# Performance work log

Hardware: AMD Instinct MI355X
Metric: run time of the kernel (lower is better)

The kernel has to match this reference:

```python
import jax, jax.numpy as jnp
import numpy as np

# Qwen3-VL-MoE text experts (training path): token permute -> grouped GEMM
# (gate_up) -> SwiGLU -> grouped GEMM (down) -> token unpermute + prob combine.
# Routing is generated perfectly balanced (each expert receives exactly M/E
# expanded tokens) so the grouped GEMM over the sorted token buffer is exactly
# a batched matmul over E contiguous groups -- same math as npu_grouped_matmul.

E, H, D, T, K = 32, 2048, 768, 4096, 8  # experts, hidden, moe_intermediate, tokens, top_k
M = T * K                                # expanded rows


def setup_inputs() -> dict:
    key = jax.random.key(0)
    k1, k2, k3, k4, k5 = jax.random.split(key, 5)
    hidden_states = jax.random.normal(k1, (T, H), dtype=jnp.float32)
    routing_weights = jax.nn.softmax(jax.random.normal(k2, (T, E), dtype=jnp.float32), axis=-1)
    # balanced expert assignment: each expert id appears exactly M // E times
    flat = jnp.tile(jnp.arange(E, dtype=jnp.int32), M // E)
    router_indices = jax.random.permutation(k3, flat).reshape(T, K)
    gate_up_proj = jax.random.normal(k4, (E, H, 2 * D), dtype=jnp.float32) * 0.02
    down_proj = jax.random.normal(k5, (E, D, H), dtype=jnp.float32) * 0.02
    return {
        "hidden_states": hidden_states,
        "routing_weights": routing_weights,
        "router_indices": router_indices,
        "gate_up_proj": gate_up_proj,
        "down_proj": down_proj,
    }


def reference(hidden_states, routing_weights, router_indices, gate_up_proj, down_proj):
    n_tok, hid = hidden_states.shape
    n_exp = gate_up_proj.shape[0]
    top_k = router_indices.shape[1]
    n_rows = n_tok * top_k
    grp = n_rows // n_exp  # balanced group size

    # --- npu_moe_token_permute: sort expanded (token, slot) rows by expert id
    flat_experts = router_indices.reshape(-1)            # (M,)
    order = jnp.argsort(flat_experts)                    # stable sort by expert
    permuted = hidden_states[order // top_k]             # (M, H)

    # --- grouped GEMM #1 (gate_up): balanced groups -> batched matmul
    xg = permuted.reshape(n_exp, grp, hid)               # (E, g, H)
    gate_up = jnp.einsum('egh,ehd->egd', xg, gate_up_proj)  # (E, g, 2D)

    # --- npu_swiglu(dim=-1): silu(first half) * second half
    gate, up = jnp.split(gate_up, 2, axis=-1)
    act = jax.nn.silu(gate) * up                         # (E, g, D)

    # --- grouped GEMM #2 (down)
    out = jnp.einsum('egd,edh->egh', act, down_proj).reshape(n_rows, hid)

    # --- npu_moe_token_unpermute: invert permutation, combine with probs
    inv = jnp.argsort(order)
    expanded = out[inv].reshape(n_tok, top_k, hid)       # (T, K, H)
    probs = jnp.take_along_axis(routing_weights, router_indices, axis=1)  # (T, K)
    return jnp.einsum('tkh,tk->th', expanded, probs)     # (T, H)
```

## Files before the change

### kernel.cpp

```cpp
#include <hip/hip_runtime.h>
#include <hip/hip_bf16.h>
#include <cstdint>


#define E_   32
#define H_   2048
#define D_   768
#define T_   4096
#define K_   8
#define M_   (T_ * K_)
#define G_   (M_ / E_)
#define GU2  (2 * D_)

typedef unsigned short u16;
typedef short bf16x8 __attribute__((ext_vector_type(8)));
typedef float f32x4 __attribute__((ext_vector_type(4)));
typedef unsigned short u16x2 __attribute__((ext_vector_type(2)));
typedef unsigned short u16x8 __attribute__((ext_vector_type(8)));

__device__ __forceinline__ u16 f2bf(float f) {
  unsigned u = __float_as_uint(f);
  u += 0x7FFFu + ((u >> 16) & 1u);
  return (u16)(u >> 16);
}
__device__ __forceinline__ float bf2f(u16 v) {
  return __uint_as_float(((unsigned)v) << 16);
}

#define GLOAD16(g, l) __builtin_amdgcn_global_load_lds(                        \
    (const __attribute__((address_space(1))) void*)(g),                        \
    (__attribute__((address_space(3))) void*)(l), 16, 0, 0)

#define VM4()   asm volatile("s_waitcnt vmcnt(4)" ::: "memory")
#define VM0()   asm volatile("s_waitcnt vmcnt(0)" ::: "memory")
#define LGKM0() asm volatile("s_waitcnt lgkmcnt(0)" ::: "memory")
#define SCHB()  __builtin_amdgcn_sched_barrier(0)
#define BAR()   __builtin_amdgcn_s_barrier()

__global__ __launch_bounds__(256) void cvt_hidden(const float* __restrict__ in,
                                                  u16* __restrict__ out) {
  const int i = blockIdx.x * 256 + threadIdx.x;
  const float4 v = ((const float4*)in)[i];
  u16x2 a; a.x = f2bf(v.x); a.y = f2bf(v.y);
  u16x2 b; b.x = f2bf(v.z); b.y = f2bf(v.w);
  *(u16x2*)&out[(size_t)i * 4]     = a;
  *(u16x2*)&out[(size_t)i * 4 + 2] = b;
}

__global__ __launch_bounds__(256) void transpose_cvt(const float* __restrict__ in,
                                                     u16* __restrict__ out,
                                                     int R, int C, int mode) {
  __shared__ u16 tl[64][65];
  const int b = blockIdx.z;
  const int c0 = blockIdx.x * 64, r0 = blockIdx.y * 64;
  const float* ip = in + ((size_t)b * R + r0) * C + c0;
  const int lr = threadIdx.x >> 6;
  const int lc = threadIdx.x & 63;
#pragma unroll
  for (int p = 0; p < 16; ++p) {
    const int r = p * 4 + lr;
    tl[r][lc] = f2bf(ip[(size_t)r * C + lc]);
  }
  __syncthreads();
  const int wr = threadIdx.x >> 5;
  const int wi = threadIdx.x & 31;
#pragma unroll
  for (int p = 0; p < 8; ++p) {
    const int c = p * 8 + wr;
    const int gc = c0 + c;
    int rr;
    if (mode == 1) {
      const int j = (gc < D_) ? gc : (gc - D_);
      rr = (j >> 4) * 32 + ((gc < D_) ? 0 : 16) + (j & 15);
    } else {
      rr = gc;
    }
    u16x2 v; v.x = tl[2 * wi][c]; v.y = tl[2 * wi + 1][c];
    *(u16x2*)&out[((size_t)b * C + rr) * R + r0 + 2 * wi] = v;
  }
}

__global__ __launch_bounds__(256) void build_perm(const int* __restrict__ ridx,
                                                  int* __restrict__ perm_src) {
  const int e = blockIdx.x;
  const int lane = threadIdx.x & 63, wid = threadIdx.x >> 6;
  __shared__ int wcnt[4];
  __shared__ int running;
  if (threadIdx.x == 0) running = 0;
  __syncthreads();
  for (int base = 0; base < M_; base += 256) {
    const int i = base + threadIdx.x;
    const bool match = (ridx[i] == e);
    const unsigned long long mask = __ballot(match);
    if (lane == 0) wcnt[wid] = __popcll(mask);
    __syncthreads();
    int wpre = 0;
    for (int w0 = 0; w0 < wid; ++w0) wpre += wcnt[w0];
    const int rank = __popcll(mask & ((1ull << lane) - 1ull));
    if (match) perm_src[e * G_ + running + wpre + rank] = i;
    __syncthreads();
    if (threadIdx.x == 0) running += wcnt[0] + wcnt[1] + wcnt[2] + wcnt[3];
    __syncthreads();
  }
}

__global__ __launch_bounds__(256) void gather_probs(const int* __restrict__ ridx,
                                                    const float* __restrict__ rw,
                                                    float* __restrict__ probs) {
  const int i = blockIdx.x * 256 + threadIdx.x;
  const int t = i >> 3;
  probs[i] = rw[t * E_ + ridx[i]];
}

__global__ __launch_bounds__(512, 2) void gemm1_swiglu(
    const u16* __restrict__ hid, const u16* __restrict__ gup,
    const int* __restrict__ perm, u16* __restrict__ act) {
  __shared__ u16 As[4][8192];
  __shared__ u16 Bs[4][8192];
  const int NT = H_ / 32;

  const int nwg = 6 * 4 * E_;
  const int wid = (blockIdx.x % 8) * (nwg / 8) + blockIdx.x / 8;
  const int e = wid / 24;
  const int mb = (wid / 6) % 4;
  const int nb = wid % 6;

  const int tid = threadIdx.x;
  const int lane = tid & 63, w = tid >> 6;
  const int wr = w >> 2, wc = w & 3;

  const int srow = tid >> 2, schunk = tid & 3;
  const u16* pA[2]; const u16* pB[2];
#pragma unroll
  for (int q = 0; q < 2; ++q) {
    const int r = q * 128 + srow;
    const int cg = (schunk ^ ((r >> 1) & 3)) * 8;
    const int token = perm[e * G_ + mb * 256 + r] >> 3;
    pA[q] = hid + (size_t)token * H_ + cg;
    pB[q] = gup + ((size_t)e * GU2 + nb * 256 + r) * H_ + cg;
  }

  int aoff[8], boff[4];
  {
    const int l15 = lane & 15, hk = lane >> 4;
#pragma unroll
    for (int m = 0; m < 8; ++m) {
      const int rA = wr * 128 + m * 16 + l15;
      aoff[m] = rA * 32 + ((hk ^ ((rA >> 1) & 3)) * 8);
    }
#pragma unroll
    for (int n = 0; n < 4; ++n) {
      const int rB = wc * 64 + n * 16 + l15;
      boff[n] = rB * 32 + ((hk ^ ((rB >> 1) & 3)) * 8);
    }
  }

  f32x4 acc[8][4];
#pragma unroll
  for (int m = 0; m < 8; ++m)
#pragma unroll
    for (int n = 0; n < 4; ++n) acc[m][n] = (f32x4){0.f, 0.f, 0.f, 0.f};

  GLOAD16(pA[0], &As[0][tid * 8]);      GLOAD16(pA[1], &As[0][4096 + tid * 8]);
  GLOAD16(pB[0], &Bs[0][tid * 8]);      GLOAD16(pB[1], &Bs[0][4096 + tid * 8]);
  GLOAD16(pA[0] + 32, &As[1][tid * 8]); GLOAD16(pA[1] + 32, &As[1][4096 + tid * 8]);
  GLOAD16(pB[0] + 32, &Bs[1][tid * 8]); GLOAD16(pB[1] + 32, &Bs[1][4096 + tid * 8]);
  VM4(); BAR(); SCHB();

#pragma unroll 4
  for (int t = 0; t < NT; ++t) {
    const int slot = t & 3, ts = (t + 2) & 3;
    const bool st = (t + 2) < NT;
    const u16* Ab = As[slot]; const u16* Bb = Bs[slot];
    bf16x8 av[4], bv[4];
#pragma unroll
    for (int n = 0; n < 4; ++n) bv[n] = *(const bf16x8*)&Bb[boff[n]];
#pragma unroll
    for (int m = 0; m < 4; ++m) av[m] = *(const bf16x8*)&Ab[aoff[m]];
    if (st) {
      GLOAD16(pA[0] + (t + 2) * 32, &As[ts][tid * 8]);
      GLOAD16(pA[1] + (t + 2) * 32, &As[ts][4096 + tid * 8]);
    }
    SCHB(); BAR(); LGKM0(); SCHB();
    __builtin_amdgcn_s_setprio(1);
#pragma unroll
    for (int m = 0; m < 4; ++m)
#pragma unroll
      for (int n = 0; n < 4; ++n)
        acc[m][n] = __builtin_amdgcn_mfma_f32_16x16x32_bf16(av[m], bv[n],
                                                            acc[m][n], 0, 0, 0);
    __builtin_amdgcn_s_setprio(0);
    SCHB(); BAR();
#pragma unroll
    for (int m = 0; m < 4; ++m) av[m] = *(const bf16x8*)&Ab[aoff[m + 4]];
    if (st) {
      GLOAD16(pB[0] + (t + 2) * 32, &Bs[ts][tid * 8]);
      GLOAD16(pB[1] + (t + 2) * 32, &Bs[ts][4096 + tid * 8]);
    }
    SCHB(); BAR(); LGKM0(); SCHB();
    __builtin_amdgcn_s_setprio(1);
#pragma unroll
    for (int m = 0; m < 4; ++m)
#pragma unroll
      for (int n = 0; n < 4; ++n)
        acc[m + 4][n] = __builtin_amdgcn_mfma_f32_16x16x32_bf16(av[m], bv[n],
                                                                acc[m + 4][n], 0, 0, 0);
    __builtin_amdgcn_s_setprio(0);
    SCHB();
    if (st) { VM4(); } else { VM0(); }
    BAR();
  }

  const int lrow = (lane >> 4) * 4, lcol = lane & 15;
#pragma unroll
  for (int m = 0; m < 8; ++m)
#pragma unroll
    for (int p = 0; p < 2; ++p)
#pragma unroll
      for (int r = 0; r < 4; ++r) {
        const float g = acc[m][2 * p][r];
        const float u = acc[m][2 * p + 1][r];
        const float a_ = g / (1.f + __expf(-g)) * u;
        const int row = mb * 256 + wr * 128 + m * 16 + lrow + r;
        const int dcol = (nb * 8 + wc * 2 + p) * 16 + lcol;
        act[((size_t)e * G_ + row) * D_ + dcol] = f2bf(a_);
      }
}

__global__ __launch_bounds__(512, 2) void gemm2_scatter(
    const u16* __restrict__ act, const u16* __restrict__ dwn,
    const int* __restrict__ perm, u16* __restrict__ expo) {
  __shared__ u16 As[4][8192];
  __shared__ u16 Bs[4][8192];
  const int NT = D_ / 32;

  const int nwg = 8 * 4 * E_;
  const int wid = (blockIdx.x % 8) * (nwg / 8) + blockIdx.x / 8;
  const int e = wid / 32;
  const int mb = (wid / 8) % 4;
  const int nb = wid % 8;

  const int tid = threadIdx.x;
  const int lane = tid & 63, w = tid >> 6;
  const int wr = w >> 2, wc = w & 3;

  const int srow = tid >> 2, schunk = tid & 3;
  const u16* pA[2]; const u16* pB[2];
#pragma unroll
  for (int q = 0; q < 2; ++q) {
    const int r = q * 128 + srow;
    const int cg = (schunk ^ ((r >> 1) & 3)) * 8;
    pA[q] = act + ((size_t)e * G_ + mb * 256 + r) * D_ + cg;
    pB[q] = dwn + ((size_t)e * H_ + nb * 256 + r) * D_ + cg;
  }

  int aoff[8], boff[4];
  {
    const int l15 = lane & 15, hk = lane >> 4;
#pragma unroll
    for (int m = 0; m < 8; ++m) {
      const int rA = wr * 128 + m * 16 + l15;
      aoff[m] = rA * 32 + ((hk ^ ((rA >> 1) & 3)) * 8);
    }
#pragma unroll
    for (int n = 0; n < 4; ++n) {
      const int rB = wc * 64 + n * 16 + l15;
      boff[n] = rB * 32 + ((hk ^ ((rB >> 1) & 3)) * 8);
    }
  }

  f32x4 acc[8][4];
#pragma unroll
  for (int m = 0; m < 8; ++m)
#pragma unroll
    for (int n = 0; n < 4; ++n) acc[m][n] = (f32x4){0.f, 0.f, 0.f, 0.f};

  GLOAD16(pA[0], &As[0][tid * 8]);      GLOAD16(pA[1], &As[0][4096 + tid * 8]);
  GLOAD16(pB[0], &Bs[0][tid * 8]);      GLOAD16(pB[1], &Bs[0][4096 + tid * 8]);
  GLOAD16(pA[0] + 32, &As[1][tid * 8]); GLOAD16(pA[1] + 32, &As[1][4096 + tid * 8]);
  GLOAD16(pB[0] + 32, &Bs[1][tid * 8]); GLOAD16(pB[1] + 32, &Bs[1][4096 + tid * 8]);
  VM4(); BAR(); SCHB();

#pragma unroll 4
  for (int t = 0; t < NT; ++t) {
    const int slot = t & 3, ts = (t + 2) & 3;
    const bool st = (t + 2) < NT;
    const u16* Ab = As[slot]; const u16* Bb = Bs[slot];
    bf16x8 av[4], bv[4];
#pragma unroll
    for (int n = 0; n < 4; ++n) bv[n] = *(const bf16x8*)&Bb[boff[n]];
#pragma unroll
    for (int m = 0; m < 4; ++m) av[m] = *(const bf16x8*)&Ab[aoff[m]];
    if (st) {
      GLOAD16(pA[0] + (t + 2) * 32, &As[ts][tid * 8]);
      GLOAD16(pA[1] + (t + 2) * 32, &As[ts][4096 + tid * 8]);
    }
    SCHB(); BAR(); LGKM0(); SCHB();
    __builtin_amdgcn_s_setprio(1);
#pragma unroll
    for (int m = 0; m < 4; ++m)
#pragma unroll
      for (int n = 0; n < 4; ++n)
        acc[m][n] = __builtin_amdgcn_mfma_f32_16x16x32_bf16(av[m], bv[n],
                                                            acc[m][n], 0, 0, 0);
    __builtin_amdgcn_s_setprio(0);
    SCHB(); BAR();
#pragma unroll
    for (int m = 0; m < 4; ++m) av[m] = *(const bf16x8*)&Ab[aoff[m + 4]];
    if (st) {
      GLOAD16(pB[0] + (t + 2) * 32, &Bs[ts][tid * 8]);
      GLOAD16(pB[1] + (t + 2) * 32, &Bs[ts][4096 + tid * 8]);
    }
    SCHB(); BAR(); LGKM0(); SCHB();
    __builtin_amdgcn_s_setprio(1);
#pragma unroll
    for (int m = 0; m < 4; ++m)
#pragma unroll
      for (int n = 0; n < 4; ++n)
        acc[m + 4][n] = __builtin_amdgcn_mfma_f32_16x16x32_bf16(av[m], bv[n],
                                                                acc[m + 4][n], 0, 0, 0);
    __builtin_amdgcn_s_setprio(0);
    SCHB();
    if (st) { VM4(); } else { VM0(); }
    BAR();
  }

  const int lrow = (lane >> 4) * 4, lcol = lane & 15;
#pragma unroll
  for (int m = 0; m < 8; ++m)
#pragma unroll
    for (int r = 0; r < 4; ++r) {
      const int dst = e * G_ + mb * 256 + wr * 128 + m * 16 + lrow + r;
      const int src = perm[dst];
      u16* orow = expo + (size_t)src * H_ + nb * 256 + wc * 64;
#pragma unroll
      for (int n = 0; n < 4; ++n)
        orow[n * 16 + lcol] = f2bf(acc[m][n][r]);
    }
}

__global__ __launch_bounds__(256) void combine(const u16* __restrict__ expo,
                                               const float* __restrict__ probs,
                                               float* __restrict__ out) {
  const int t = blockIdx.x;
  const int h0 = threadIdx.x * 8;
  float r[8] = {0.f, 0.f, 0.f, 0.f, 0.f, 0.f, 0.f, 0.f};
#pragma unroll
  for (int k = 0; k < K_; ++k) {
    const float p = probs[t * K_ + k];
    const u16x8 v = *(const u16x8*)&expo[((size_t)(t * K_ + k)) * H_ + h0];
#pragma unroll
    for (int j = 0; j < 8; ++j) r[j] += p * bf2f(v[j]);
  }
  float4 o0 = {r[0], r[1], r[2], r[3]};
  float4 o1 = {r[4], r[5], r[6], r[7]};
  *(float4*)&out[(size_t)t * H_ + h0]     = o0;
  *(float4*)&out[(size_t)t * H_ + h0 + 4] = o1;
}

extern "C" void kernel_launch(void* const* d_in, const int* in_sizes, int n_in,
                              void* d_out, int out_size, void* d_ws, size_t ws_size,
                              hipStream_t stream) {
  const float* hidden = (const float*)d_in[0];
  const float* rw     = (const float*)d_in[1];
  const int*   ridx   = (const int*)d_in[2];
  const float* gup_f  = (const float*)d_in[3];
  const float* dwn_f  = (const float*)d_in[4];
  float* out = (float*)d_out;

  char* ws = (char*)d_ws;
  size_t off = 0;
  auto alloc = [&](size_t bytes) -> void* {
    void* p = ws + off;
    off += (bytes + 255) & ~(size_t)255;
    return p;
  };
  u16*   hid_bf = (u16*)alloc((size_t)T_ * H_ * 2);
  u16*   gup_t  = (u16*)alloc((size_t)E_ * GU2 * H_ * 2);
  u16*   dwn_t  = (u16*)alloc((size_t)E_ * H_ * D_ * 2);
  u16*   act    = (u16*)alloc((size_t)M_ * D_ * 2);
  u16*   expo   = (u16*)alloc((size_t)M_ * H_ * 2);
  int*   perm   = (int*)alloc((size_t)M_ * 4);
  float* probs  = (float*)alloc((size_t)M_ * 4);
  if (off > ws_size) return;

  cvt_hidden<<<(T_ * H_ / 4) / 256, 256, 0, stream>>>(hidden, hid_bf);
  transpose_cvt<<<dim3(GU2 / 64, H_ / 64, E_), 256, 0, stream>>>(gup_f, gup_t, H_, GU2, 1);
  transpose_cvt<<<dim3(H_ / 64, D_ / 64, E_), 256, 0, stream>>>(dwn_f, dwn_t, D_, H_, 0);
  build_perm<<<E_, 256, 0, stream>>>(ridx, perm);
  gather_probs<<<M_ / 256, 256, 0, stream>>>(ridx, rw, probs);
  gemm1_swiglu<<<6 * 4 * E_, 512, 0, stream>>>(hid_bf, gup_t, perm, act);
  gemm2_scatter<<<8 * 4 * E_, 512, 0, stream>>>(act, dwn_t, perm, expo);
  combine<<<T_, 256, 0, stream>>>(expo, probs, out);
}
```

Before: 620.0 us.

## Deepen GEMM prefetch to three stages and vectorize transpose-convert kernel

Both grouped GEMM kernels now prefetch three K-tiles ahead instead of two, using the fourth LDS ring slot, with waitcnt thresholds adjusted so up to eight loads stay in flight. This is meant to hide more global memory latency behind the MFMA work. Separately, the weight transpose-convert kernel now reads float4 rows, stores transposed into a padded LDS tile, and writes 16-byte vectors instead of 4-byte pairs. The deeper pipeline adds more outstanding loads and more complex tail waits.

```diff
diff --git a/kernel.cpp b/kernel.cpp
--- a/kernel.cpp
+++ b/kernel.cpp
@@ -31,6 +31,7 @@
     (const __attribute__((address_space(1))) void*)(g),                        \
     (__attribute__((address_space(3))) void*)(l), 16, 0, 0)
 
+#define VM8()   asm volatile("s_waitcnt vmcnt(8)" ::: "memory")
 #define VM4()   asm volatile("s_waitcnt vmcnt(4)" ::: "memory")
 #define VM0()   asm volatile("s_waitcnt vmcnt(0)" ::: "memory")
 #define LGKM0() asm volatile("s_waitcnt lgkmcnt(0)" ::: "memory")
@@ -50,23 +51,27 @@
 __global__ __launch_bounds__(256) void transpose_cvt(const float* __restrict__ in,
                                                      u16* __restrict__ out,
                                                      int R, int C, int mode) {
-  __shared__ u16 tl[64][65];
+  __shared__ u16 tl[64 * 72];
   const int b = blockIdx.z;
   const int c0 = blockIdx.x * 64, r0 = blockIdx.y * 64;
+  const int tid = threadIdx.x;
   const float* ip = in + ((size_t)b * R + r0) * C + c0;
-  const int lr = threadIdx.x >> 6;
-  const int lc = threadIdx.x & 63;
-#pragma unroll
-  for (int p = 0; p < 16; ++p) {
-    const int r = p * 4 + lr;
-    tl[r][lc] = f2bf(ip[(size_t)r * C + lc]);
+  const int rr4 = tid >> 4;
+  const int cc4 = (tid & 15) * 4;
+#pragma unroll
+  for (int p = 0; p < 4; ++p) {
+    const int r = p * 16 + rr4;
+    const float4 v = *(const float4*)&ip[(size_t)r * C + cc4];
+    tl[(cc4 + 0) * 72 + r] = f2bf(v.x);
+    tl[(cc4 + 1) * 72 + r] = f2bf(v.y);
+    tl[(cc4 + 2) * 72 + r] = f2bf(v.z);
+    tl[(cc4 + 3) * 72 + r] = f2bf(v.w);
   }
   __syncthreads();
-  const int wr = threadIdx.x >> 5;
-  const int wi = threadIdx.x & 31;
-#pragma unroll
-  for (int p = 0; p < 8; ++p) {
-    const int c = p * 8 + wr;
+  const int rs = (tid & 7) * 8;
+#pragma unroll
+  for (int q = 0; q < 2; ++q) {
+    const int c = q * 32 + (tid >> 3);
     const int gc = c0 + c;
     int rr;
     if (mode == 1) {
@@ -75,8 +80,8 @@
     } else {
       rr = gc;
     }
-    u16x2 v; v.x = tl[2 * wi][c]; v.y = tl[2 * wi + 1][c];
-    *(u16x2*)&out[((size_t)b * C + rr) * R + r0 + 2 * wi] = v;
+    const u16x8 v = *(const u16x8*)&tl[c * 72 + rs];
+    *(u16x8*)&out[((size_t)b * C + rr) * R + r0 + rs] = v;
   }
 }
 
@@ -165,12 +170,14 @@
   GLOAD16(pB[0], &Bs[0][tid * 8]);      GLOAD16(pB[1], &Bs[0][4096 + tid * 8]);
   GLOAD16(pA[0] + 32, &As[1][tid * 8]); GLOAD16(pA[1] + 32, &As[1][4096 + tid * 8]);
   GLOAD16(pB[0] + 32, &Bs[1][tid * 8]); GLOAD16(pB[1] + 32, &Bs[1][4096 + tid * 8]);
-  VM4(); BAR(); SCHB();
+  GLOAD16(pA[0] + 64, &As[2][tid * 8]); GLOAD16(pA[1] + 64, &As[2][4096 + tid * 8]);
+  GLOAD16(pB[0] + 64, &Bs[2][tid * 8]); GLOAD16(pB[1] + 64, &Bs[2][4096 + tid * 8]);
+  VM8(); BAR(); SCHB();
 
 #pragma unroll 4
   for (int t = 0; t < NT; ++t) {
-    const int slot = t & 3, ts = (t + 2) & 3;
-    const bool st = (t + 2) < NT;
+    const int slot = t & 3, ts = (t + 3) & 3;
+    const bool st = (t + 3) < NT;
     const u16* Ab = As[slot]; const u16* Bb = Bs[slot];
     bf16x8 av[4], bv[4];
 #pragma unroll
@@ -178,8 +185,8 @@
 #pragma unroll
     for (int m = 0; m < 4; ++m) av[m] = *(const bf16x8*)&Ab[aoff[m]];
     if (st) {
-      GLOAD16(pA[0] + (t + 2) * 32, &As[ts][tid * 8]);
-      GLOAD16(pA[1] + (t + 2) * 32, &As[ts][4096 + tid * 8]);
+      GLOAD16(pA[0] + (t + 3) * 32, &As[ts][tid * 8]);
+      GLOAD16(pA[1] + (t + 3) * 32, &As[ts][4096 + tid * 8]);
     }
     SCHB(); BAR(); LGKM0(); SCHB();
     __builtin_amdgcn_s_setprio(1);
@@ -194,8 +201,8 @@
 #pragma unroll
     for (int m = 0; m < 4; ++m) av[m] = *(const bf16x8*)&Ab[aoff[m + 4]];
     if (st) {
-      GLOAD16(pB[0] + (t + 2) * 32, &Bs[ts][tid * 8]);
-      GLOAD16(pB[1] + (t + 2) * 32, &Bs[ts][4096 + tid * 8]);
+      GLOAD16(pB[0] + (t + 3) * 32, &Bs[ts][tid * 8]);
+      GLOAD16(pB[1] + (t + 3) * 32, &Bs[ts][4096 + tid * 8]);
     }
     SCHB(); BAR(); LGKM0(); SCHB();
     __builtin_amdgcn_s_setprio(1);
@@ -207,7 +214,9 @@
                                                                 acc[m + 4][n], 0, 0, 0);
     __builtin_amdgcn_s_setprio(0);
     SCHB();
-    if (st) { VM4(); } else { VM0(); }
+    if (t + 3 < NT)      { VM8(); }
+    else if (t + 2 < NT) { VM4(); }
+    else                 { VM0(); }
     BAR();
   }
 
@@ -279,12 +288,14 @@
   GLOAD16(pB[0], &Bs[0][tid * 8]);      GLOAD16(pB[1], &Bs[0][4096 + tid * 8]);
   GLOAD16(pA[0] + 32, &As[1][tid * 8]); GLOAD16(pA[1] + 32, &As[1][4096 + tid * 8]);
   GLOAD16(pB[0] + 32, &Bs[1][tid * 8]); GLOAD16(pB[1] + 32, &Bs[1][4096 + tid * 8]);
-  VM4(); BAR(); SCHB();
+  GLOAD16(pA[0] + 64, &As[2][tid * 8]); GLOAD16(pA[1] + 64, &As[2][4096 + tid * 8]);
+  GLOAD16(pB[0] + 64, &Bs[2][tid * 8]); GLOAD16(pB[1] + 64, &Bs[2][4096 + tid * 8]);
+  VM8(); BAR(); SCHB();
 
 #pragma unroll 4
   for (int t = 0; t < NT; ++t) {
-    const int slot = t & 3, ts = (t + 2) & 3;
-    const bool st = (t + 2) < NT;
+    const int slot = t & 3, ts = (t + 3) & 3;
+    const bool st = (t + 3) < NT;
     const u16* Ab = As[slot]; const u16* Bb = Bs[slot];
     bf16x8 av[4], bv[4];
 #pragma unroll
@@ -292,8 +303,8 @@
 #pragma unroll
     for (int m = 0; m < 4; ++m) av[m] = *(const bf16x8*)&Ab[aoff[m]];
     if (st) {
-      GLOAD16(pA[0] + (t + 2) * 32, &As[ts][tid * 8]);
-      GLOAD16(pA[1] + (t + 2) * 32, &As[ts][4096 + tid * 8]);
+      GLOAD16(pA[0] + (t + 3) * 32, &As[ts][tid * 8]);
+      GLOAD16(pA[1] + (t + 3) * 32, &As[ts][4096 + tid * 8]);
     }
     SCHB(); BAR(); LGKM0(); SCHB();
     __builtin_amdgcn_s_setprio(1);
@@ -308,8 +319,8 @@
 #pragma unroll
     for (int m = 0; m < 4; ++m) av[m] = *(const bf16x8*)&Ab[aoff[m + 4]];
     if (st) {
-      GLOAD16(pB[0] + (t + 2) * 32, &Bs[ts][tid * 8]);
-      GLOAD16(pB[1] + (t + 2) * 32, &Bs[ts][4096 + tid * 8]);
+      GLOAD16(pB[0] + (t + 3) * 32, &Bs[ts][tid * 8]);
+      GLOAD16(pB[1] + (t + 3) * 32, &Bs[ts][4096 + tid * 8]);
     }
     SCHB(); BAR(); LGKM0(); SCHB();
     __builtin_amdgcn_s_setprio(1);
@@ -321,7 +332,9 @@
                                                                 acc[m + 4][n], 0, 0, 0);
     __builtin_amdgcn_s_setprio(0);
     SCHB();
-    if (st) { VM4(); } else { VM0(); }
+    if (t + 3 < NT)      { VM8(); }
+    else if (t + 2 < NT) { VM4(); }
+    else                 { VM0(); }
     BAR();
   }
 
```

Result: no change. 618.6 us (-0.2%).
